# Optimization experiments

Hardware: AMD Instinct MI355X
Metric: run time of the kernel (lower is better)

The kernel has to match this reference:

```python
import jax, jax.numpy as jnp
import numpy as np
import math

H = 16
DQ = 64
NEG = -1000000000.0


def setup_inputs() -> dict:
    key = jax.random.key(0)
    ks = jax.random.split(key, 8)
    B, S, D = 2, 2048, 1024
    scale = 1.0 / math.sqrt(D)
    return {
        "embedding": jax.random.normal(ks[0], (B, S, D), dtype=jnp.float32),
        "mask": jax.random.randint(ks[1], (B, 1, S), 0, 2, dtype=jnp.int32),
        "Wq": jax.random.normal(ks[2], (D, D), dtype=jnp.float32) * scale,
        "bq": jnp.zeros((D,), dtype=jnp.float32),
        "Wk": jax.random.normal(ks[3], (D, D), dtype=jnp.float32) * scale,
        "bk": jnp.zeros((D,), dtype=jnp.float32),
        "Wv": jax.random.normal(ks[4], (D, D), dtype=jnp.float32) * scale,
        "bv": jnp.zeros((D,), dtype=jnp.float32),
        "Wo": jax.random.normal(ks[5], (D, D), dtype=jnp.float32) * scale,
        "bo": jnp.zeros((D,), dtype=jnp.float32),
    }


def reference(embedding, mask, Wq, bq, Wk, bk, Wv, bv, Wo, bo):
    B, S, D = embedding.shape
    # projections -> [B, H, S, DQ]
    def proj(W, b):
        return (embedding @ W + b).reshape(B, S, H, DQ).transpose(0, 2, 1, 3)
    q, k, v = proj(Wq, bq), proj(Wk, bk), proj(Wv, bv)
    scores = jnp.einsum("bhqd,bhkd->bhqk", q, k) / math.sqrt(DQ)
    m = mask[:, None]  # [B,1,1,S] broadcasts over heads and query positions
    scores = jnp.where(m == 0, NEG, scores)
    attn = jax.nn.softmax(scores, axis=-1)
    x = jnp.einsum("bhqk,bhkd->bhqd", attn, v)
    x = x.transpose(0, 2, 1, 3).reshape(B, S, H * DQ)
    return x @ Wo + bo
```

## Files before the change

kernel.cpp:

```cpp
#include <hip/hip_runtime.h>
#include <stdint.h>

#define B_ 2
#define S_ 2048
#define D_ 1024
#define H_ 16
#define DQ_ 64
#define M_ 4096
#define CLOG2 16.0f
#define NEGB -1000000000.0f

typedef unsigned short ushort_t;
typedef __attribute__((ext_vector_type(8))) short short8;
typedef __attribute__((ext_vector_type(4))) float floatx4;

#if __has_builtin(__builtin_amdgcn_exp2f)
#define EXP2(x) __builtin_amdgcn_exp2f(x)
#else
#define EXP2(x) exp2f(x)
#endif

__device__ __forceinline__ ushort_t f2bf(float f) {
  union { float f; uint32_t u; } v; v.f = f;
  uint32_t r = v.u + 0x7FFFu + ((v.u >> 16) & 1u);
  return (ushort_t)(r >> 16);
}

__device__ __forceinline__ void async16(const ushort_t* g, ushort_t* l) {
  __builtin_amdgcn_global_load_lds(
      (const __attribute__((address_space(1))) uint32_t*)g,
      (__attribute__((address_space(3))) uint32_t*)l, 16, 0, 0);
}


__global__ void k_cvt_emb(const float* __restrict__ in, ushort_t* __restrict__ out) {
  int i = (blockIdx.x * 256 + threadIdx.x) * 4;
  float4 v = *(const float4*)(in + i);
  uint64_t pk = (uint64_t)f2bf(v.x) | ((uint64_t)f2bf(v.y) << 16) |
                ((uint64_t)f2bf(v.z) << 32) | ((uint64_t)f2bf(v.w) << 48);
  *(uint64_t*)(out + i) = pk;
}

__global__ void k_cvt_w(const float* __restrict__ Wq, const float* __restrict__ Wk,
                        const float* __restrict__ Wv, const float* __restrict__ Wo,
                        ushort_t* __restrict__ Wt) {
  const float* W = (blockIdx.z == 0) ? Wq : (blockIdx.z == 1) ? Wk
                 : (blockIdx.z == 2) ? Wv : Wo;
  ushort_t* out = Wt + (size_t)blockIdx.z * D_ * D_;
  __shared__ float t[32][33];
  int k0 = blockIdx.x * 32, n0 = blockIdx.y * 32;
  int tx = threadIdx.x, ty = threadIdx.y;
  for (int r = 0; r < 32; r += 8)
    t[ty + r][tx] = W[(size_t)(k0 + ty + r) * D_ + n0 + tx];
  __syncthreads();
  for (int r = 0; r < 32; r += 8)
    out[(size_t)(n0 + ty + r) * D_ + k0 + tx] = f2bf(t[tx][ty + r]);
}

template <int IM>
__device__ __forceinline__ void gemm_core2(const ushort_t* __restrict__ A,
                                           const ushort_t* __restrict__ Bt,
                                           ushort_t* As, ushort_t* Bs,
                                           int m0, int n0, floatx4 (&acc)[IM][4]) {
  int t = threadIdx.x, lane = t & 63, w = t >> 6;
  int wm = (w >> 1) * (IM * 16), wn = (w & 1) * 64;
  int l15 = lane & 15, quad = lane >> 4;
  int srow8 = (lane >> 3) & 7;
  int sch = ((lane & 7) ^ srow8) * 8;
  const ushort_t* Ag = A + (size_t)(m0 + w * 8 + srow8) * D_ + sch;
  const ushort_t* Bg = Bt + (size_t)(n0 + w * 8 + srow8) * D_ + sch;
  for (int kt = 0; kt < D_; kt += 64) {
    __syncthreads();
#pragma unroll
    for (int c = 0; c < IM; c++)
      async16(Ag + kt + (size_t)c * 32 * D_, As + (c * 32 + w * 8) * 64);
#pragma unroll
    for (int c = 0; c < 4; c++)
      async16(Bg + kt + (size_t)c * 32 * D_, Bs + (c * 32 + w * 8) * 64);
    __syncthreads();
#pragma unroll
    for (int ks = 0; ks < 2; ks++) {
      int ch = ((ks * 4 + quad) ^ (l15 & 7)) * 8;
      short8 a[IM], b[4];
#pragma unroll
      for (int i = 0; i < IM; i++)
        a[i] = *(const short8*)(As + (wm + i * 16 + l15) * 64 + ch);
#pragma unroll
      for (int j = 0; j < 4; j++)
        b[j] = *(const short8*)(Bs + (wn + j * 16 + l15) * 64 + ch);
#pragma unroll
      for (int i = 0; i < IM; i++)
#pragma unroll
        for (int j = 0; j < 4; j++)
          acc[i][j] = __builtin_amdgcn_mfma_f32_16x16x32_bf16(a[i], b[j], acc[i][j], 0, 0, 0);
    }
  }
}

__global__ __launch_bounds__(256, 3) void k_proj(
    const ushort_t* __restrict__ A, const ushort_t* __restrict__ Wt,
    const float* __restrict__ bq, const float* __restrict__ bk,
    const float* __restrict__ bv,
    ushort_t* __restrict__ Q, ushort_t* __restrict__ K, ushort_t* __restrict__ V) {
  __shared__ __align__(16) ushort_t As[128 * 64];
  __shared__ __align__(16) ushort_t Bs[128 * 64];
  int z = blockIdx.z;
  const ushort_t* Bt = Wt + (size_t)z * D_ * D_;
  const float* bias = (z == 0) ? bq : (z == 1) ? bk : bv;
  int m0 = blockIdx.x * 128, n0 = blockIdx.y * 128;
  floatx4 acc[4][4] = {};
  gemm_core2<4>(A, Bt, As, Bs, m0, n0, acc);
  int lane = threadIdx.x & 63, w = threadIdx.x >> 6;
  int wm = (w >> 1) * 64, wn = (w & 1) * 64;
  int quad = lane >> 4, l15 = lane & 15;
  float scale = (z == 0) ? 0.125f * 1.44269504f : 1.0f;
#pragma unroll
  for (int i = 0; i < 4; i++)
#pragma unroll
    for (int j = 0; j < 4; j++) {
      int ncol = n0 + wn + j * 16 + l15;
      float bb = bias[ncol];
      int h = ncol >> 6, dq = ncol & 63;
      int m = m0 + wm + i * 16 + quad * 4;
      int b = m >> 11, s = m & (S_ - 1);
      if (z == 2) {
        uint64_t pk = (uint64_t)f2bf(acc[i][j][0] + bb) |
                      ((uint64_t)f2bf(acc[i][j][1] + bb) << 16) |
                      ((uint64_t)f2bf(acc[i][j][2] + bb) << 32) |
                      ((uint64_t)f2bf(acc[i][j][3] + bb) << 48);
        *(uint64_t*)(V + ((size_t)(b * H_ + h) * DQ_ + dq) * S_ + s) = pk;
      } else {
        ushort_t* dst = (z == 0) ? Q : K;
#pragma unroll
        for (int r = 0; r < 4; r++)
          dst[((size_t)(b * H_ + h) * S_ + (s + r)) * DQ_ + dq] =
              f2bf((acc[i][j][r] + bb) * scale);
      }
    }
}

__global__ __launch_bounds__(256, 2) void k_attn(
    const ushort_t* __restrict__ Q, const ushort_t* __restrict__ Kg,
    const ushort_t* __restrict__ Vt, const int* __restrict__ mask,
    ushort_t* __restrict__ X) {
  int bh = blockIdx.y, b = bh >> 4, h = bh & 15;
  int q0 = blockIdx.x * 128;
  int t = threadIdx.x, lane = t & 63, w = t >> 6;
  int quad = lane >> 4, l15 = lane & 15;
  const ushort_t* Qh = Q + (size_t)bh * S_ * DQ_;
  const ushort_t* Kh = Kg + (size_t)bh * S_ * DQ_;
  const ushort_t* Vh = Vt + (size_t)bh * DQ_ * S_;
  const int* mb = mask + b * S_;

  __shared__ __align__(16) ushort_t Ks[64 * 64];
  __shared__ __align__(16) ushort_t Vs[64 * 64];
  __shared__ __align__(16) ushort_t Ps[4][32 * 72];
  __shared__ float biasS[S_];

  for (int i = t; i < S_; i += 256) biasS[i] = mb[i] ? -CLOG2 : NEGB;

  short8 qf[2][2];
#pragma unroll
  for (int i = 0; i < 2; i++)
#pragma unroll
    for (int ks = 0; ks < 2; ks++)
      qf[i][ks] = *(const short8*)(Qh + (size_t)(q0 + w * 32 + i * 16 + l15) * DQ_ +
                                   ks * 32 + quad * 8);

  int srow8 = (lane >> 3) & 7;
  int sch = ((lane & 7) ^ srow8) * 8;
  const ushort_t* Kg1 = Kh + (size_t)(w * 8 + srow8) * DQ_ + sch;
  const ushort_t* Vg1 = Vh + (size_t)(w * 8 + srow8) * S_ + sch;

  floatx4 o[2][4] = {};
  float lpart[2][4] = {};

  for (int k0 = 0; k0 < S_; k0 += 64) {
    __syncthreads();
    async16(Kg1 + (size_t)k0 * DQ_, Ks + w * 512);
    async16(Kg1 + (size_t)(k0 + 32) * DQ_, Ks + w * 512 + 2048);
    async16(Vg1 + k0, Vs + w * 512);
    async16(Vg1 + (size_t)32 * S_ + k0, Vs + w * 512 + 2048);
    __syncthreads();

    floatx4 sacc[2][4] = {};
#pragma unroll
    for (int ks = 0; ks < 2; ks++) {
      int ch = ((ks * 4 + quad) ^ (l15 & 7)) * 8;
      short8 kf[4];
#pragma unroll
      for (int j = 0; j < 4; j++)
        kf[j] = *(const short8*)(Ks + (j * 16 + l15) * 64 + ch);
#pragma unroll
      for (int i = 0; i < 2; i++)
#pragma unroll
        for (int j = 0; j < 4; j++)
          sacc[i][j] = __builtin_amdgcn_mfma_f32_16x16x32_bf16(qf[i][ks], kf[j], sacc[i][j], 0, 0, 0);
    }

    float bj[4];
#pragma unroll
    for (int j = 0; j < 4; j++) bj[j] = biasS[k0 + j * 16 + l15];

    ushort_t* Pw = Ps[w];
#pragma unroll
    for (int i = 0; i < 2; i++)
#pragma unroll
      for (int r = 0; r < 4; r++) {
        float ps = 0.0f;
#pragma unroll
        for (int j = 0; j < 4; j++) {
          float p = EXP2(sacc[i][j][r] + bj[j]);
          sacc[i][j][r] = p;
          ps += p;
          Pw[(i * 16 + quad * 4 + r) * 72 + j * 16 + l15] = f2bf(p);
        }
        lpart[i][r] += ps;
      }

#pragma unroll
    for (int ks = 0; ks < 2; ks++) {
      int ch = ((ks * 4 + quad) ^ (l15 & 7)) * 8;
      short8 pf[2], vf[4];
#pragma unroll
      for (int i = 0; i < 2; i++)
        pf[i] = *(const short8*)(Pw + (i * 16 + l15) * 72 + ks * 32 + quad * 8);
#pragma unroll
      for (int jo = 0; jo < 4; jo++)
        vf[jo] = *(const short8*)(Vs + (jo * 16 + l15) * 64 + ch);
#pragma unroll
      for (int i = 0; i < 2; i++)
#pragma unroll
        for (int jo = 0; jo < 4; jo++)
          o[i][jo] = __builtin_amdgcn_mfma_f32_16x16x32_bf16(pf[i], vf[jo], o[i][jo], 0, 0, 0);
    }
  }

#pragma unroll
  for (int i = 0; i < 2; i++)
#pragma unroll
    for (int r = 0; r < 4; r++) {
      float l = lpart[i][r];
      for (int d = 1; d < 16; d <<= 1) l += __shfl_xor(l, d, 64);
      float inv = 1.0f / l;
      int qrow = q0 + w * 32 + i * 16 + quad * 4 + r;
      size_t base = ((size_t)(b * S_ + qrow)) * D_ + h * DQ_;
#pragma unroll
      for (int jo = 0; jo < 4; jo++)
        X[base + jo * 16 + l15] = f2bf(o[i][jo][r] * inv);
    }
}

__global__ __launch_bounds__(256, 2) void k_oproj(
    const ushort_t* __restrict__ A, const ushort_t* __restrict__ Wt,
    const float* __restrict__ bias, float* __restrict__ C) {
  __shared__ __align__(16) ushort_t As[64 * 64];
  __shared__ __align__(16) ushort_t Bs[128 * 64];
  int m0 = blockIdx.x * 64, n0 = blockIdx.y * 128;
  floatx4 acc[2][4] = {};
  gemm_core2<2>(A, Wt, As, Bs, m0, n0, acc);
  int lane = threadIdx.x & 63, w = threadIdx.x >> 6;
  int wm = (w >> 1) * 32, wn = (w & 1) * 64;
  int quad = lane >> 4, l15 = lane & 15;
#pragma unroll
  for (int i = 0; i < 2; i++)
#pragma unroll
    for (int j = 0; j < 4; j++) {
      int ncol = n0 + wn + j * 16 + l15;
      float bb = bias[ncol];
      int mr = m0 + wm + i * 16 + quad * 4;
#pragma unroll
      for (int r = 0; r < 4; r++)
        C[(size_t)(mr + r) * D_ + ncol] = acc[i][j][r] + bb;
    }
}

extern "C" void kernel_launch(void* const* d_in, const int* in_sizes, int n_in,
                              void* d_out, int out_size, void* d_ws, size_t ws_size,
                              hipStream_t stream) {
  const float* emb  = (const float*)d_in[0];
  const int*   mask = (const int*)d_in[1];
  const float* Wq = (const float*)d_in[2];
  const float* bq = (const float*)d_in[3];
  const float* Wk = (const float*)d_in[4];
  const float* bk = (const float*)d_in[5];
  const float* Wv = (const float*)d_in[6];
  const float* bv = (const float*)d_in[7];
  const float* Wo = (const float*)d_in[8];
  const float* bo = (const float*)d_in[9];
  float* out = (float*)d_out;

  ushort_t* embb = (ushort_t*)d_ws;
  ushort_t* Wt   = embb + (size_t)M_ * D_;
  ushort_t* Qb   = Wt + (size_t)4 * D_ * D_;
  ushort_t* Kb   = Qb + (size_t)M_ * D_;
  ushort_t* Vb   = Kb + (size_t)M_ * D_;
  ushort_t* Xb   = Vb + (size_t)M_ * D_;

  k_cvt_emb<<<dim3(M_ * D_ / 1024), 256, 0, stream>>>(emb, embb);
  k_cvt_w<<<dim3(32, 32, 4), dim3(32, 8), 0, stream>>>(Wq, Wk, Wv, Wo, Wt);
  k_proj<<<dim3(32, 8, 3), 256, 0, stream>>>(embb, Wt, bq, bk, bv, Qb, Kb, Vb);
  k_attn<<<dim3(16, 32), 256, 0, stream>>>(Qb, Kb, Vb, mask, Xb);
  k_oproj<<<dim3(64, 8), 256, 0, stream>>>(Xb, Wt + (size_t)3 * D_ * D_, bo, out);
}
```

Before: 210.4 us.

## Halve attention query tile to 64 rows and read mask directly from global

The attention kernel now handles 64 query rows per block (16 per wave) instead of 128, doubling the grid to 1024 blocks and raising launch bounds to 4 blocks per CU. The shared-memory bias table is dropped; mask values are loaded from global memory inside the key loop. The aim is more occupancy and better spread across CUs on a machine with many compute units. In exchange, each K/V tile loaded into shared memory now feeds half as many MFMAs, so global K/V traffic doubles, and mask loads go to global/cache on every iteration.

```diff
diff --git a/kernel.cpp b/kernel.cpp
--- a/kernel.cpp
+++ b/kernel.cpp
@@ -139,12 +139,12 @@
     }
 }
 
-__global__ __launch_bounds__(256, 2) void k_attn(
+__global__ __launch_bounds__(256, 4) void k_attn(
     const ushort_t* __restrict__ Q, const ushort_t* __restrict__ Kg,
     const ushort_t* __restrict__ Vt, const int* __restrict__ mask,
     ushort_t* __restrict__ X) {
   int bh = blockIdx.y, b = bh >> 4, h = bh & 15;
-  int q0 = blockIdx.x * 128;
+  int q0 = blockIdx.x * 64;
   int t = threadIdx.x, lane = t & 63, w = t >> 6;
   int quad = lane >> 4, l15 = lane & 15;
   const ushort_t* Qh = Q + (size_t)bh * S_ * DQ_;
@@ -154,26 +154,21 @@
 
   __shared__ __align__(16) ushort_t Ks[64 * 64];
   __shared__ __align__(16) ushort_t Vs[64 * 64];
-  __shared__ __align__(16) ushort_t Ps[4][32 * 72];
-  __shared__ float biasS[S_];
-
-  for (int i = t; i < S_; i += 256) biasS[i] = mb[i] ? -CLOG2 : NEGB;
-
-  short8 qf[2][2];
-#pragma unroll
-  for (int i = 0; i < 2; i++)
-#pragma unroll
-    for (int ks = 0; ks < 2; ks++)
-      qf[i][ks] = *(const short8*)(Qh + (size_t)(q0 + w * 32 + i * 16 + l15) * DQ_ +
-                                   ks * 32 + quad * 8);
+  __shared__ __align__(16) ushort_t Ps[4][16 * 72];
+
+  short8 qf[2];
+#pragma unroll
+  for (int ks = 0; ks < 2; ks++)
+    qf[ks] = *(const short8*)(Qh + (size_t)(q0 + w * 16 + l15) * DQ_ +
+                              ks * 32 + quad * 8);
 
   int srow8 = (lane >> 3) & 7;
   int sch = ((lane & 7) ^ srow8) * 8;
   const ushort_t* Kg1 = Kh + (size_t)(w * 8 + srow8) * DQ_ + sch;
   const ushort_t* Vg1 = Vh + (size_t)(w * 8 + srow8) * S_ + sch;
 
-  floatx4 o[2][4] = {};
-  float lpart[2][4] = {};
+  floatx4 o[4] = {};
+  float lpart[4] = {};
 
   for (int k0 = 0; k0 < S_; k0 += 64) {
     __syncthreads();
@@ -183,7 +178,7 @@
     async16(Vg1 + (size_t)32 * S_ + k0, Vs + w * 512 + 2048);
     __syncthreads();
 
-    floatx4 sacc[2][4] = {};
+    floatx4 sacc[4] = {};
 #pragma unroll
     for (int ks = 0; ks < 2; ks++) {
       int ch = ((ks * 4 + quad) ^ (l15 & 7)) * 8;
@@ -192,63 +187,53 @@
       for (int j = 0; j < 4; j++)
         kf[j] = *(const short8*)(Ks + (j * 16 + l15) * 64 + ch);
 #pragma unroll
-      for (int i = 0; i < 2; i++)
-#pragma unroll
-        for (int j = 0; j < 4; j++)
-          sacc[i][j] = __builtin_amdgcn_mfma_f32_16x16x32_bf16(qf[i][ks], kf[j], sacc[i][j], 0, 0, 0);
+      for (int j = 0; j < 4; j++)
+        sacc[j] = __builtin_amdgcn_mfma_f32_16x16x32_bf16(qf[ks], kf[j], sacc[j], 0, 0, 0);
     }
 
     float bj[4];
 #pragma unroll
-    for (int j = 0; j < 4; j++) bj[j] = biasS[k0 + j * 16 + l15];
+    for (int j = 0; j < 4; j++)
+      bj[j] = mb[k0 + j * 16 + l15] ? -CLOG2 : NEGB;
 
     ushort_t* Pw = Ps[w];
 #pragma unroll
-    for (int i = 0; i < 2; i++)
-#pragma unroll
-      for (int r = 0; r < 4; r++) {
-        float ps = 0.0f;
-#pragma unroll
-        for (int j = 0; j < 4; j++) {
-          float p = EXP2(sacc[i][j][r] + bj[j]);
-          sacc[i][j][r] = p;
-          ps += p;
-          Pw[(i * 16 + quad * 4 + r) * 72 + j * 16 + l15] = f2bf(p);
-        }
-        lpart[i][r] += ps;
+    for (int r = 0; r < 4; r++) {
+      float ps = 0.0f;
+#pragma unroll
+      for (int j = 0; j < 4; j++) {
+        float p = EXP2(sacc[j][r] + bj[j]);
+        ps += p;
+        Pw[(quad * 4 + r) * 72 + j * 16 + l15] = f2bf(p);
       }
+      lpart[r] += ps;
+    }
 
 #pragma unroll
     for (int ks = 0; ks < 2; ks++) {
       int ch = ((ks * 4 + quad) ^ (l15 & 7)) * 8;
-      short8 pf[2], vf[4];
-#pragma unroll
-      for (int i = 0; i < 2; i++)
-        pf[i] = *(const short8*)(Pw + (i * 16 + l15) * 72 + ks * 32 + quad * 8);
+      short8 pf, vf[4];
+      pf = *(const short8*)(Pw + l15 * 72 + ks * 32 + quad * 8);
 #pragma unroll
       for (int jo = 0; jo < 4; jo++)
         vf[jo] = *(const short8*)(Vs + (jo * 16 + l15) * 64 + ch);
 #pragma unroll
-      for (int i = 0; i < 2; i++)
-#pragma unroll
-        for (int jo = 0; jo < 4; jo++)
-          o[i][jo] = __builtin_amdgcn_mfma_f32_16x16x32_bf16(pf[i], vf[jo], o[i][jo], 0, 0, 0);
+      for (int jo = 0; jo < 4; jo++)
+        o[jo] = __builtin_amdgcn_mfma_f32_16x16x32_bf16(pf, vf[jo], o[jo], 0, 0, 0);
     }
   }
 
 #pragma unroll
-  for (int i = 0; i < 2; i++)
-#pragma unroll
-    for (int r = 0; r < 4; r++) {
-      float l = lpart[i][r];
-      for (int d = 1; d < 16; d <<= 1) l += __shfl_xor(l, d, 64);
-      float inv = 1.0f / l;
-      int qrow = q0 + w * 32 + i * 16 + quad * 4 + r;
-      size_t base = ((size_t)(b * S_ + qrow)) * D_ + h * DQ_;
-#pragma unroll
-      for (int jo = 0; jo < 4; jo++)
-        X[base + jo * 16 + l15] = f2bf(o[i][jo][r] * inv);
-    }
+  for (int r = 0; r < 4; r++) {
+    float l = lpart[r];
+    for (int d = 1; d < 16; d <<= 1) l += __shfl_xor(l, d, 64);
+    float inv = 1.0f / l;
+    int qrow = q0 + w * 16 + quad * 4 + r;
+    size_t base = ((size_t)(b * S_ + qrow)) * D_ + h * DQ_;
+#pragma unroll
+    for (int jo = 0; jo < 4; jo++)
+      X[base + jo * 16 + l15] = f2bf(o[jo][r] * inv);
+  }
 }
 
 __global__ __launch_bounds__(256, 2) void k_oproj(
@@ -300,6 +285,6 @@
   k_cvt_emb<<<dim3(M_ * D_ / 1024), 256, 0, stream>>>(emb, embb);
   k_cvt_w<<<dim3(32, 32, 4), dim3(32, 8), 0, stream>>>(Wq, Wk, Wv, Wo, Wt);
   k_proj<<<dim3(32, 8, 3), 256, 0, stream>>>(embb, Wt, bq, bk, bv, Qb, Kb, Vb);
-  k_attn<<<dim3(16, 32), 256, 0, stream>>>(Qb, Kb, Vb, mask, Xb);
+  k_attn<<<dim3(32, 32), 256, 0, stream>>>(Qb, Kb, Vb, mask, Xb);
   k_oproj<<<dim3(64, 8), 256, 0, stream>>>(Xb, Wt + (size_t)3 * D_ * D_, bo, out);
 }
```

New measurement: 210.8 us. Within noise of the previous version (+0.2%).
